# Optimization experiments

Hardware: AMD Instinct MI355X
Metric: run time of the kernel (lower is better)

## Reference

```python
import jax, jax.numpy as jnp
import numpy as np

VOCAB, E, H = 53, 16, 32
B, S = 4096, 512


def setup_inputs() -> dict:
    key = jax.random.key(0)
    k = jax.random.split(key, 8)
    x = jax.random.randint(k[0], (B, S), 0, VOCAB)
    emb = jax.random.normal(k[1], (VOCAB, E), jnp.float32) * 0.1
    emb = emb.at[0].set(0.0)  # padding_idx=0 row is zero
    s = 1.0 / np.sqrt(H).astype(np.float32)
    W_ih = jax.random.uniform(k[2], (4 * H, E), jnp.float32, -s, s)
    W_hh = jax.random.uniform(k[3], (4 * H, H), jnp.float32, -s, s)
    b_ih = jax.random.uniform(k[4], (4 * H,), jnp.float32, -s, s)
    b_hh = jax.random.uniform(k[5], (4 * H,), jnp.float32, -s, s)
    sf = 1.0 / np.sqrt(H).astype(np.float32)
    W_fc = jax.random.uniform(k[6], (1, H), jnp.float32, -sf, sf)
    b_fc = jax.random.uniform(k[7], (1,), jnp.float32, -sf, sf)
    return {"x": x, "emb": emb, "W_ih": W_ih, "W_hh": W_hh,
            "b_ih": b_ih, "b_hh": b_hh, "W_fc": W_fc, "b_fc": b_fc}


def _lstm_last_hidden(ex, W_ih, W_hh, b_ih, b_hh):
    # ex: [B,S,E]. Precompute input contribution to all 4 gates: [B,S,4H]
    xg = jnp.einsum('bse,ge->bsg', ex, W_ih) + (b_ih + b_hh)
    b = ex.shape[0]
    h0 = jnp.zeros((b, H), ex.dtype)
    c0 = jnp.zeros((b, H), ex.dtype)

    def step(carry, xt):
        h, c = carry
        g = xt + h @ W_hh.T  # [B,4H]; torch gate order i,f,g,o
        i, f, gg, o = jnp.split(g, 4, axis=-1)
        c = jax.nn.sigmoid(f) * c + jax.nn.sigmoid(i) * jnp.tanh(gg)
        h = jax.nn.sigmoid(o) * jnp.tanh(c)
        return (h, c), None

    (hT, _), _ = jax.lax.scan(step, (h0, c0), jnp.swapaxes(xg, 0, 1))
    return hT  # [B,H]


def reference(x, emb, W_ih, W_hh, b_ih, b_hh, W_fc, b_fc):
    ex = emb[x]  # [B,S,E] embedding lookup
    hT = _lstm_last_hidden(ex, W_ih, W_hh, b_ih, b_hh)
    out = hT @ W_fc.T + b_fc  # [B,1]
    return jax.nn.sigmoid(out).squeeze()  # [B]
```

## Files before the change

### kernel.cpp

```cpp
#include <hip/hip_runtime.h>

#define VOCAB 53
#define EDIM  16
#define H     32
#define SEQ   512
#define BATCH 4096
#define LOG2E 1.4426950408889634f
#define XRS   132
#define HS    72
#define RSC   2048.0f
#define RSCI  (1.0f/2048.0f)

typedef _Float16 f16x8 __attribute__((ext_vector_type(8)));
typedef float f32x4 __attribute__((ext_vector_type(4)));

__device__ __forceinline__ float exp2_hw(float x) {
    float r; asm("v_exp_f32 %0, %1" : "=v"(r) : "v"(x)); return r;
}
__device__ __forceinline__ float sig_exp2(float xs) {
    return __builtin_amdgcn_rcpf(1.0f + exp2_hw(xs));
}

__device__ __forceinline__ void decode_row(int rp, int& orig, float& scale) {
    int m = rp >> 4, rem = rp & 15, s = rem >> 2, g = rem & 3;
    orig = g * 32 + 4 * m + s;
    scale = (g == 2) ? (-2.0f * LOG2E) : (-LOG2E);
}

__global__ __launch_bounds__(512, 1)
void lstm_seq_classifier(const int* __restrict__ x,
                         const float* __restrict__ emb,
                         const float* __restrict__ W_ih,
                         const float* __restrict__ W_hh,
                         const float* __restrict__ b_ih,
                         const float* __restrict__ b_hh,
                         const float* __restrict__ W_fc,
                         const float* __restrict__ b_fc,
                         float* __restrict__ out) {
    __shared__ float xg_perm[VOCAB * XRS];
    __shared__ _Float16 whi[128 * 32];
    __shared__ _Float16 wlo[128 * 32];
    __shared__ __align__(16) _Float16 hhi_buf[2][16][HS];
    __shared__ __align__(16) _Float16 hlo_buf[2][16][HS];
    __shared__ float red[16 * 33];

    const int tid  = threadIdx.x;
    const int lane = tid & 63;
    const int w    = tid >> 6;
    const int col  = lane & 15;
    const int q    = lane >> 4;

    for (int idx = tid; idx < VOCAB * 128; idx += 512) {
        int v = idx >> 7, rp = idx & 127;
        int orig; float scale; decode_row(rp, orig, scale);
        float acc = b_ih[orig] + b_hh[orig];
        const float* ev = emb + v * EDIM;
        const float* wr = W_ih + orig * EDIM;
#pragma unroll
        for (int e = 0; e < EDIM; ++e) acc += ev[e] * wr[e];
        xg_perm[v * XRS + rp] = scale * acc;
    }
    for (int idx = tid; idx < 128 * 32; idx += 512) {
        int rp = idx >> 5, k = idx & 31;
        int orig; float scale; decode_row(rp, orig, scale);
        float wv = scale * W_hh[orig * H + k];
        _Float16 hi = (_Float16)wv;
        whi[idx] = hi;
        wlo[idx] = (_Float16)((wv - (float)hi) * RSC);
    }
    for (int idx = tid; idx < 2 * 16 * HS; idx += 512) {
        (&hhi_buf[0][0][0])[idx] = (_Float16)0.f;
        (&hlo_buf[0][0][0])[idx] = (_Float16)0.f;
    }
    __syncthreads();

    const f16x8 Ahi = *reinterpret_cast<const f16x8*>(&whi[(16 * w + col) * 32 + 8 * q]);
    const f16x8 Alo = *reinterpret_cast<const f16x8*>(&wlo[(16 * w + col) * 32 + 8 * q]);

    const long xb = (long)(blockIdx.x * 16 + col) * SEQ;
    int vb = x[xb];
    int vc = x[xb + 1];
    f32x4 xg_cur = *reinterpret_cast<const f32x4*>(&xg_perm[vb * XRS + 16 * w + 4 * q]);

    float c = 0.0f, h = 0.0f;

    for (int s = 0; s < SEQ; ++s) {
        int vn = x[xb + ((s + 2) & (SEQ - 1))];
        f32x4 xg_nxt = *reinterpret_cast<const f32x4*>(
            &xg_perm[vc * XRS + 16 * w + 4 * q]);
        const int rb = s & 1;
        f16x8 Bhi = *reinterpret_cast<const f16x8*>(&hhi_buf[rb][col][8 * q]);
        f16x8 Blo = *reinterpret_cast<const f16x8*>(&hlo_buf[rb][col][8 * q]);

        f32x4 D  = __builtin_amdgcn_mfma_f32_16x16x32_f16(Ahi, Bhi, xg_cur, 0, 0, 0);
        f32x4 Dr = __builtin_amdgcn_mfma_f32_16x16x32_f16(Alo, Bhi,
                       f32x4{0.f, 0.f, 0.f, 0.f}, 0, 0, 0);
        Dr = __builtin_amdgcn_mfma_f32_16x16x32_f16(Ahi, Blo, Dr, 0, 0, 0);
        float zi = __builtin_fmaf(RSCI, Dr[0], D[0]);
        float zf = __builtin_fmaf(RSCI, Dr[1], D[1]);
        float zg = __builtin_fmaf(RSCI, Dr[2], D[2]);
        float zo = __builtin_fmaf(RSCI, Dr[3], D[3]);

        float si = sig_exp2(zi);
        float sf = sig_exp2(zf);
        float ug = sig_exp2(zg);
        float so = sig_exp2(zo);
        float gt = __builtin_fmaf(2.0f, ug, -1.0f);
        c = __builtin_fmaf(sf, c, si * gt);
        float tc = __builtin_fmaf(2.0f, sig_exp2(-2.0f * LOG2E * c), -1.0f);
        h = so * tc;

        const int nb = (s + 1) & 1;
        _Float16 hh = (_Float16)h;
        hhi_buf[nb][col][4 * w + q] = hh;
        hlo_buf[nb][col][4 * w + q] = (_Float16)((h - (float)hh) * RSC);
        __syncthreads();
        xg_cur = xg_nxt;
        vc = vn;
    }

    red[col * 33 + 4 * w + q] = h * W_fc[4 * w + q];
    __syncthreads();
    if (w == 0) {
        const float* rr = &red[col * 33];
        float p = 0.f;
#pragma unroll
        for (int u = 0; u < 8; ++u) p += rr[8 * q + u] ;
        p += __shfl_xor(p, 16);
        p += __shfl_xor(p, 32);
        if (lane < 16) {
            out[blockIdx.x * 16 + col] = sig_exp2(-LOG2E * (p + b_fc[0]));
        }
    }
}

extern "C" void kernel_launch(void* const* d_in, const int* in_sizes, int n_in,
                              void* d_out, int out_size, void* d_ws, size_t ws_size,
                              hipStream_t stream) {
    const int*   x    = (const int*)d_in[0];
    const float* emb  = (const float*)d_in[1];
    const float* W_ih = (const float*)d_in[2];
    const float* W_hh = (const float*)d_in[3];
    const float* b_ih = (const float*)d_in[4];
    const float* b_hh = (const float*)d_in[5];
    const float* W_fc = (const float*)d_in[6];
    const float* b_fc = (const float*)d_in[7];
    float* out = (float*)d_out;

    dim3 grid(BATCH / 16);
    dim3 block(512);
    lstm_seq_classifier<<<grid, block, 0, stream>>>(x, emb, W_ih, W_hh,
                                                    b_ih, b_hh, W_fc, b_fc, out);
}
```

Before: 159.4 us.

## Halve block to four waves, each computing two gate tiles per step

The block shrinks from 8 to 4 waves, and each wave now owns two 16-row gate tiles, so it issues six MFMAs per timestep. The two correction MFMAs are made independent instead of chained, and the scaling of the cell state is folded into the tanh argument. The aim is cheaper per-step barriers and more instruction-level parallelism per wave. The cost is twice the serial work per wave on the recurrence critical path.

```diff
diff --git a/kernel.cpp b/kernel.cpp
--- a/kernel.cpp
+++ b/kernel.cpp
@@ -27,7 +27,7 @@
     scale = (g == 2) ? (-2.0f * LOG2E) : (-LOG2E);
 }
 
-__global__ __launch_bounds__(512, 1)
+__global__ __launch_bounds__(256, 1)
 void lstm_seq_classifier(const int* __restrict__ x,
                          const float* __restrict__ emb,
                          const float* __restrict__ W_ih,
@@ -50,7 +50,7 @@
     const int col  = lane & 15;
     const int q    = lane >> 4;
 
-    for (int idx = tid; idx < VOCAB * 128; idx += 512) {
+    for (int idx = tid; idx < VOCAB * 128; idx += 256) {
         int v = idx >> 7, rp = idx & 127;
         int orig; float scale; decode_row(rp, orig, scale);
         float acc = b_ih[orig] + b_hh[orig];
@@ -60,7 +60,7 @@
         for (int e = 0; e < EDIM; ++e) acc += ev[e] * wr[e];
         xg_perm[v * XRS + rp] = scale * acc;
     }
-    for (int idx = tid; idx < 128 * 32; idx += 512) {
+    for (int idx = tid; idx < 128 * 32; idx += 256) {
         int rp = idx >> 5, k = idx & 31;
         int orig; float scale; decode_row(rp, orig, scale);
         float wv = scale * W_hh[orig * H + k];
@@ -68,64 +68,94 @@
         whi[idx] = hi;
         wlo[idx] = (_Float16)((wv - (float)hi) * RSC);
     }
-    for (int idx = tid; idx < 2 * 16 * HS; idx += 512) {
+    for (int idx = tid; idx < 2 * 16 * HS; idx += 256) {
         (&hhi_buf[0][0][0])[idx] = (_Float16)0.f;
         (&hlo_buf[0][0][0])[idx] = (_Float16)0.f;
     }
     __syncthreads();
 
-    const f16x8 Ahi = *reinterpret_cast<const f16x8*>(&whi[(16 * w + col) * 32 + 8 * q]);
-    const f16x8 Alo = *reinterpret_cast<const f16x8*>(&wlo[(16 * w + col) * 32 + 8 * q]);
+    const int c0 = w, c1 = w + 4;
+    const f16x8 Ahi0 = *reinterpret_cast<const f16x8*>(&whi[(16 * c0 + col) * 32 + 8 * q]);
+    const f16x8 Alo0 = *reinterpret_cast<const f16x8*>(&wlo[(16 * c0 + col) * 32 + 8 * q]);
+    const f16x8 Ahi1 = *reinterpret_cast<const f16x8*>(&whi[(16 * c1 + col) * 32 + 8 * q]);
+    const f16x8 Alo1 = *reinterpret_cast<const f16x8*>(&wlo[(16 * c1 + col) * 32 + 8 * q]);
 
     const long xb = (long)(blockIdx.x * 16 + col) * SEQ;
-    int vb = x[xb];
+    const int xo0 = 16 * c0 + 4 * q;
+    const int xo1 = 16 * c1 + 4 * q;
     int vc = x[xb + 1];
-    f32x4 xg_cur = *reinterpret_cast<const f32x4*>(&xg_perm[vb * XRS + 16 * w + 4 * q]);
+    {
+    }
+    const int v0 = x[xb];
+    f32x4 xg_cur0 = *reinterpret_cast<const f32x4*>(&xg_perm[v0 * XRS + xo0]);
+    f32x4 xg_cur1 = *reinterpret_cast<const f32x4*>(&xg_perm[v0 * XRS + xo1]);
 
-    float c = 0.0f, h = 0.0f;
+    const int u0 = 4 * c0 + q;
+    const int u1 = 4 * c1 + q;
+
+    float ccs0 = 0.0f, h0 = 0.0f;
+    float ccs1 = 0.0f, h1 = 0.0f;
+    const f32x4 zeroC = {0.f, 0.f, 0.f, 0.f};
 
     for (int s = 0; s < SEQ; ++s) {
         int vn = x[xb + ((s + 2) & (SEQ - 1))];
-        f32x4 xg_nxt = *reinterpret_cast<const f32x4*>(
-            &xg_perm[vc * XRS + 16 * w + 4 * q]);
-        const int rb = s & 1;
+        f32x4 xg_nxt0 = *reinterpret_cast<const f32x4*>(
+            &xg_perm[vc * XRS + xo0]);
+        f32x4 xg_nxt1 = *reinterpret_cast<const f32x4*>(
+            &xg_perm[vc * XRS + xo1]);
+        const int rb = s & 1, nb = rb ^ 1;
         f16x8 Bhi = *reinterpret_cast<const f16x8*>(&hhi_buf[rb][col][8 * q]);
         f16x8 Blo = *reinterpret_cast<const f16x8*>(&hlo_buf[rb][col][8 * q]);
 
-        f32x4 D  = __builtin_amdgcn_mfma_f32_16x16x32_f16(Ahi, Bhi, xg_cur, 0, 0, 0);
-        f32x4 Dr = __builtin_amdgcn_mfma_f32_16x16x32_f16(Alo, Bhi,
-                       f32x4{0.f, 0.f, 0.f, 0.f}, 0, 0, 0);
-        Dr = __builtin_amdgcn_mfma_f32_16x16x32_f16(Ahi, Blo, Dr, 0, 0, 0);
-        float zi = __builtin_fmaf(RSCI, Dr[0], D[0]);
-        float zf = __builtin_fmaf(RSCI, Dr[1], D[1]);
-        float zg = __builtin_fmaf(RSCI, Dr[2], D[2]);
-        float zo = __builtin_fmaf(RSCI, Dr[3], D[3]);
+        f32x4 D0   = __builtin_amdgcn_mfma_f32_16x16x32_f16(Ahi0, Bhi, xg_cur0, 0, 0, 0);
+        f32x4 Dra0 = __builtin_amdgcn_mfma_f32_16x16x32_f16(Alo0, Bhi, zeroC, 0, 0, 0);
+        f32x4 Drb0 = __builtin_amdgcn_mfma_f32_16x16x32_f16(Ahi0, Blo, zeroC, 0, 0, 0);
+        f32x4 D1   = __builtin_amdgcn_mfma_f32_16x16x32_f16(Ahi1, Bhi, xg_cur1, 0, 0, 0);
+        f32x4 Dra1 = __builtin_amdgcn_mfma_f32_16x16x32_f16(Alo1, Bhi, zeroC, 0, 0, 0);
+        f32x4 Drb1 = __builtin_amdgcn_mfma_f32_16x16x32_f16(Ahi1, Blo, zeroC, 0, 0, 0);
 
-        float si = sig_exp2(zi);
-        float sf = sig_exp2(zf);
-        float ug = sig_exp2(zg);
-        float so = sig_exp2(zo);
-        float gt = __builtin_fmaf(2.0f, ug, -1.0f);
-        c = __builtin_fmaf(sf, c, si * gt);
-        float tc = __builtin_fmaf(2.0f, sig_exp2(-2.0f * LOG2E * c), -1.0f);
-        h = so * tc;
+        float zi0 = __builtin_fmaf(RSCI, Dra0[0] + Drb0[0], D0[0]);
+        float zf0 = __builtin_fmaf(RSCI, Dra0[1] + Drb0[1], D0[1]);
+        float zg0 = __builtin_fmaf(RSCI, Dra0[2] + Drb0[2], D0[2]);
+        float zo0 = __builtin_fmaf(RSCI, Dra0[3] + Drb0[3], D0[3]);
+        float zi1 = __builtin_fmaf(RSCI, Dra1[0] + Drb1[0], D1[0]);
+        float zf1 = __builtin_fmaf(RSCI, Dra1[1] + Drb1[1], D1[1]);
+        float zg1 = __builtin_fmaf(RSCI, Dra1[2] + Drb1[2], D1[2]);
+        float zo1 = __builtin_fmaf(RSCI, Dra1[3] + Drb1[3], D1[3]);
 
-        const int nb = (s + 1) & 1;
-        _Float16 hh = (_Float16)h;
-        hhi_buf[nb][col][4 * w + q] = hh;
-        hlo_buf[nb][col][4 * w + q] = (_Float16)((h - (float)hh) * RSC);
+        float si0 = sig_exp2(zi0), sf0 = sig_exp2(zf0);
+        float ug0 = sig_exp2(zg0), so0 = sig_exp2(zo0);
+        float si1 = sig_exp2(zi1), sf1 = sig_exp2(zf1);
+        float ug1 = sig_exp2(zg1), so1 = sig_exp2(zo1);
+
+        float t10 = __builtin_fmaf(-4.0f * LOG2E, ug0, 2.0f * LOG2E);
+        float t11 = __builtin_fmaf(-4.0f * LOG2E, ug1, 2.0f * LOG2E);
+        ccs0 = __builtin_fmaf(sf0, ccs0, si0 * t10);
+        ccs1 = __builtin_fmaf(sf1, ccs1, si1 * t11);
+        float tc0 = __builtin_fmaf(2.0f, sig_exp2(ccs0), -1.0f);
+        float tc1 = __builtin_fmaf(2.0f, sig_exp2(ccs1), -1.0f);
+        h0 = so0 * tc0;
+        h1 = so1 * tc1;
+
+        _Float16 hf0 = (_Float16)h0, hf1 = (_Float16)h1;
+        hhi_buf[nb][col][u0] = hf0;
+        hlo_buf[nb][col][u0] = (_Float16)((h0 - (float)hf0) * RSC);
+        hhi_buf[nb][col][u1] = hf1;
+        hlo_buf[nb][col][u1] = (_Float16)((h1 - (float)hf1) * RSC);
         __syncthreads();
-        xg_cur = xg_nxt;
+        xg_cur0 = xg_nxt0;
+        xg_cur1 = xg_nxt1;
         vc = vn;
     }
 
-    red[col * 33 + 4 * w + q] = h * W_fc[4 * w + q];
+    red[col * 33 + u0] = h0 * W_fc[u0];
+    red[col * 33 + u1] = h1 * W_fc[u1];
     __syncthreads();
     if (w == 0) {
         const float* rr = &red[col * 33];
         float p = 0.f;
 #pragma unroll
-        for (int u = 0; u < 8; ++u) p += rr[8 * q + u] ;
+        for (int u = 0; u < 8; ++u) p += rr[8 * q + u];
         p += __shfl_xor(p, 16);
         p += __shfl_xor(p, 32);
         if (lane < 16) {
@@ -148,7 +178,7 @@
     float* out = (float*)d_out;
 
     dim3 grid(BATCH / 16);
-    dim3 block(512);
+    dim3 block(256);
     lstm_seq_classifier<<<grid, block, 0, stream>>>(x, emb, W_ih, W_hh,
                                                     b_ih, b_hh, W_fc, b_fc, out);
 }
```

Result: slower. 192.6 us (+20.8%).

## Unroll LSTM step by two, run two blocks per CU, shorten the recurrence

Applied to the files above, without the earlier changes.

Changes launch bounds to allow two waves per EU, so two blocks can share a CU and hide each other's barrier and latency stalls. Unrolls the time loop by two with fixed buffer pointers, issues the two correction MFMAs independently instead of chaining them, and folds the cell-state scaling into c so tanh needs one fewer multiply. It also raises wave priority around the critical compute and replaces __syncthreads with an explicit lgkmcnt wait plus s_barrier. Higher occupancy caps registers per thread and may cause spills, and the fused state scaling slightly changes rounding.

```diff
diff --git a/kernel.cpp b/kernel.cpp
--- a/kernel.cpp
+++ b/kernel.cpp
@@ -27,7 +27,8 @@
     scale = (g == 2) ? (-2.0f * LOG2E) : (-LOG2E);
 }
 
-__global__ __launch_bounds__(512, 1)
+__global__ __launch_bounds__(512)
+__attribute__((amdgpu_waves_per_eu(2, 2)))
 void lstm_seq_classifier(const int* __restrict__ x,
                          const float* __restrict__ emb,
                          const float* __restrict__ W_ih,
@@ -78,46 +79,61 @@
     const f16x8 Alo = *reinterpret_cast<const f16x8*>(&wlo[(16 * w + col) * 32 + 8 * q]);
 
     const long xb = (long)(blockIdx.x * 16 + col) * SEQ;
-    int vb = x[xb];
+    const int xoff = 16 * w + 4 * q;
     int vc = x[xb + 1];
-    f32x4 xg_cur = *reinterpret_cast<const f32x4*>(&xg_perm[vb * XRS + 16 * w + 4 * q]);
+    f32x4 xg_cur = *reinterpret_cast<const f32x4*>(&xg_perm[x[xb] * XRS + xoff]);
 
-    float c = 0.0f, h = 0.0f;
+    float ccs = 0.0f, h = 0.0f;
+    const f32x4 zeroC = {0.f, 0.f, 0.f, 0.f};
 
-    for (int s = 0; s < SEQ; ++s) {
-        int vn = x[xb + ((s + 2) & (SEQ - 1))];
-        f32x4 xg_nxt = *reinterpret_cast<const f32x4*>(
-            &xg_perm[vc * XRS + 16 * w + 4 * q]);
-        const int rb = s & 1;
-        f16x8 Bhi = *reinterpret_cast<const f16x8*>(&hhi_buf[rb][col][8 * q]);
-        f16x8 Blo = *reinterpret_cast<const f16x8*>(&hlo_buf[rb][col][8 * q]);
+    const _Float16* rd_hi0 = &hhi_buf[0][col][8 * q];
+    const _Float16* rd_lo0 = &hlo_buf[0][col][8 * q];
+    const _Float16* rd_hi1 = &hhi_buf[1][col][8 * q];
+    const _Float16* rd_lo1 = &hlo_buf[1][col][8 * q];
+    _Float16* wr_hi0 = &hhi_buf[1][col][4 * w + q];
+    _Float16* wr_lo0 = &hlo_buf[1][col][4 * w + q];
+    _Float16* wr_hi1 = &hhi_buf[0][col][4 * w + q];
+    _Float16* wr_lo1 = &hlo_buf[0][col][4 * w + q];
 
-        f32x4 D  = __builtin_amdgcn_mfma_f32_16x16x32_f16(Ahi, Bhi, xg_cur, 0, 0, 0);
-        f32x4 Dr = __builtin_amdgcn_mfma_f32_16x16x32_f16(Alo, Bhi,
-                       f32x4{0.f, 0.f, 0.f, 0.f}, 0, 0, 0);
-        Dr = __builtin_amdgcn_mfma_f32_16x16x32_f16(Ahi, Blo, Dr, 0, 0, 0);
-        float zi = __builtin_fmaf(RSCI, Dr[0], D[0]);
-        float zf = __builtin_fmaf(RSCI, Dr[1], D[1]);
-        float zg = __builtin_fmaf(RSCI, Dr[2], D[2]);
-        float zo = __builtin_fmaf(RSCI, Dr[3], D[3]);
+#define STEP(S, RDHI, RDLO, WRHI, WRLO)                                       \
+    {                                                                         \
+        __builtin_amdgcn_s_setprio(1);                                        \
+        f16x8 Bhi = *reinterpret_cast<const f16x8*>(RDHI);                    \
+        f16x8 Blo = *reinterpret_cast<const f16x8*>(RDLO);                    \
+        f32x4 xg_nxt = *reinterpret_cast<const f32x4*>(                       \
+            &xg_perm[vc * XRS + xoff]);                                       \
+        int vn = x[xb + (((S) + 2) & (SEQ - 1))];                             \
+        f32x4 D   = __builtin_amdgcn_mfma_f32_16x16x32_f16(Ahi, Bhi, xg_cur, 0, 0, 0); \
+        f32x4 Dra = __builtin_amdgcn_mfma_f32_16x16x32_f16(Alo, Bhi, zeroC, 0, 0, 0);  \
+        f32x4 Drb = __builtin_amdgcn_mfma_f32_16x16x32_f16(Ahi, Blo, zeroC, 0, 0, 0);  \
+        float zi = __builtin_fmaf(RSCI, Dra[0] + Drb[0], D[0]);               \
+        float zf = __builtin_fmaf(RSCI, Dra[1] + Drb[1], D[1]);               \
+        float zg = __builtin_fmaf(RSCI, Dra[2] + Drb[2], D[2]);               \
+        float zo = __builtin_fmaf(RSCI, Dra[3] + Drb[3], D[3]);               \
+        float si = sig_exp2(zi);                                              \
+        float sf = sig_exp2(zf);                                              \
+        float ug = sig_exp2(zg);                                              \
+        float so = sig_exp2(zo);                                              \
+        float t1 = __builtin_fmaf(-4.0f * LOG2E, ug, 2.0f * LOG2E);           \
+        ccs = __builtin_fmaf(sf, ccs, si * t1);                               \
+        float so2 = so + so;                                                  \
+        float sc = sig_exp2(ccs);                                             \
+        h = __builtin_fmaf(so2, sc, -so);                                     \
+        __builtin_amdgcn_s_setprio(0);                                        \
+        _Float16 hf = (_Float16)h;                                            \
+        *(WRHI) = hf;                                                         \
+        *(WRLO) = (_Float16)((h - (float)hf) * RSC);                          \
+        asm volatile("s_waitcnt lgkmcnt(0)" ::: "memory");                    \
+        __builtin_amdgcn_s_barrier();                                         \
+        xg_cur = xg_nxt;                                                      \
+        vc = vn;                                                              \
+    }
 
-        float si = sig_exp2(zi);
-        float sf = sig_exp2(zf);
-        float ug = sig_exp2(zg);
-        float so = sig_exp2(zo);
-        float gt = __builtin_fmaf(2.0f, ug, -1.0f);
-        c = __builtin_fmaf(sf, c, si * gt);
-        float tc = __builtin_fmaf(2.0f, sig_exp2(-2.0f * LOG2E * c), -1.0f);
-        h = so * tc;
-
-        const int nb = (s + 1) & 1;
-        _Float16 hh = (_Float16)h;
-        hhi_buf[nb][col][4 * w + q] = hh;
-        hlo_buf[nb][col][4 * w + q] = (_Float16)((h - (float)hh) * RSC);
-        __syncthreads();
-        xg_cur = xg_nxt;
-        vc = vn;
+    for (int s = 0; s < SEQ; s += 2) {
+        STEP(s,     rd_hi0, rd_lo0, wr_hi0, wr_lo0)
+        STEP(s + 1, rd_hi1, rd_lo1, wr_hi1, wr_lo1)
     }
+#undef STEP
 
     red[col * 33 + 4 * w + q] = h * W_fc[4 * w + q];
     __syncthreads();
@@ -125,7 +141,7 @@
         const float* rr = &red[col * 33];
         float p = 0.f;
 #pragma unroll
-        for (int u = 0; u < 8; ++u) p += rr[8 * q + u] ;
+        for (int u = 0; u < 8; ++u) p += rr[8 * q + u];
         p += __shfl_xor(p, 16);
         p += __shfl_xor(p, 32);
         if (lane < 16) {
```

After: 170.6 us. 1.07x slower.
